# Performance work log

Hardware: AMD Instinct MI355X
Metric: run time of the kernel (lower is better)

Reference implementation:

```python
import jax, jax.numpy as jnp
import numpy as np

E = 256   # hidden_dim
H = 2     # num_heads
DH = E // H
EPS = 1e-5


def setup_inputs() -> dict:
    key = jax.random.key(0)
    ks = jax.random.split(key, 20)
    L, S, MAXLOOP = 8192, 8192, 16
    rel = jax.random.randint(ks[0], (L, MAXLOOP), 0, S)
    # sprinkle some padding sentinels (-1 / -2) like real edge loops
    pad = jax.random.uniform(ks[1], (L, MAXLOOP)) < 0.25
    rel = jnp.where(pad, -1, rel)
    rel = rel.at[:, 0].set(jnp.abs(rel[:, 0]) % S)  # ensure >=1 valid edge per face
    inp = {
        'v_face_edge_loop': rel.astype(jnp.int64) if jax.config.jax_enable_x64 else rel.astype(jnp.int32),
        'v_face_mask': jnp.ones((L,), dtype=bool),
        'v_edge_embedding': jax.random.normal(ks[2], (S, E), jnp.float32),
        'v_face_embedding': jax.random.normal(ks[3], (L, E), jnp.float32),
    }
    def w(k, shape):
        return (jax.random.normal(k, shape, jnp.float32) * 0.02)
    for i, base in ((1, 4), (2, 10)):
        inp[f'w_in{i}'] = w(ks[base + 0], (3 * E, E))
        inp[f'b_in{i}'] = jnp.zeros((3 * E,), jnp.float32)
        inp[f'w_out{i}'] = w(ks[base + 1], (E, E))
        inp[f'b_out{i}'] = jnp.zeros((E,), jnp.float32)
        inp[f'ln{i}_g'] = jnp.ones((E,), jnp.float32)
        inp[f'ln{i}_b'] = jnp.zeros((E,), jnp.float32)
    return inp


def _build_mask(face_edge_loop, S):
    # True = disallowed (torch bool attn_mask semantics).
    L = face_edge_loop.shape[0]
    rel = face_edge_loop
    invalid = (rel == -1) | (rel == -2)
    rel = jnp.where(invalid, S, rel)  # scatter invalids into sentinel column S
    mask = jnp.ones((L, S + 1), dtype=bool)
    mask = mask.at[jnp.arange(L)[:, None], rel].set(False)
    return mask[:, :S]  # [L, S]


def _mha(x, kv, mask, w_in, b_in, w_out, b_out):
    # torch nn.MultiheadAttention (unbatched, eval/no-dropout)
    wq, wk, wv = jnp.split(w_in, 3, axis=0)
    bq, bk, bv = jnp.split(b_in, 3, axis=0)
    L, S = x.shape[0], kv.shape[0]
    q = (x @ wq.T + bq).reshape(L, H, DH)
    k = (kv @ wk.T + bk).reshape(S, H, DH)
    v = (kv @ wv.T + bv).reshape(S, H, DH)
    scores = jnp.einsum('lhd,shd->hls', q, k) / np.sqrt(DH).astype(np.float32)
    scores = jnp.where(mask[None, :, :], jnp.float32(-1e9), scores)
    attn = jax.nn.softmax(scores, axis=-1)          # [H, L, S]
    out = jnp.einsum('hls,shd->lhd', attn, v).reshape(L, E)
    return out @ w_out.T + b_out


def _layernorm(x, g, b):
    m = x.mean(-1, keepdims=True)
    var = ((x - m) ** 2).mean(-1, keepdims=True)
    return (x - m) / jnp.sqrt(var + EPS) * g + b


def reference(v_face_edge_loop, v_face_mask, v_edge_embedding, v_face_embedding,
              w_in1, b_in1, w_out1, b_out1, ln1_g, ln1_b,
              w_in2, b_in2, w_out2, b_out2, ln2_g, ln2_b):
    S = v_edge_embedding.shape[0]
    # v_face_mask is all-True here (static shapes); loop[mask] == loop
    mask = _build_mask(v_face_edge_loop, S)
    x = v_face_embedding
    x = x + _mha(x, v_edge_embedding, mask, w_in1, b_in1, w_out1, b_out1)
    x = _layernorm(x, ln1_g, ln1_b)
    x = x + _mha(x, v_edge_embedding, mask, w_in2, b_in2, w_out2, b_out2)
    x = _layernorm(x, ln2_g, ln2_b)
    return x
```

## Files before the change

### kernel.cpp

```cpp
#include <hip/hip_runtime.h>
#include <hip/hip_bf16.h>

typedef short short8 __attribute__((ext_vector_type(8)));
typedef short short4v __attribute__((ext_vector_type(4)));
typedef float f32x4 __attribute__((ext_vector_type(4)));

#define E 256
#define DH 128

__device__ __forceinline__ float bf2f(__hip_bfloat16 x) { return __bfloat162float(x); }
__device__ __forceinline__ __hip_bfloat16 f2bf(float x) { return __float2bfloat16(x); }

struct CvtArgs { const float* in[6]; __hip_bfloat16* out[6]; int n[6]; };

__global__ __launch_bounds__(256) void f2b_all(CvtArgs a)
{
    int seg = blockIdx.y;
    int i = (blockIdx.x * 256 + threadIdx.x) * 8;
    if (i >= a.n[seg]) return;
    const float* in = a.in[seg];
    float4 x = *reinterpret_cast<const float4*>(in + i);
    float4 y = *reinterpret_cast<const float4*>(in + i + 4);
    __hip_bfloat16* o = a.out[seg] + i;
    o[0] = f2bf(x.x); o[1] = f2bf(x.y); o[2] = f2bf(x.z); o[3] = f2bf(x.w);
    o[4] = f2bf(y.x); o[5] = f2bf(y.y); o[6] = f2bf(y.z); o[7] = f2bf(y.w);
}

struct ProjSeg { const __hip_bfloat16* A; const __hip_bfloat16* W; const float* b; __hip_bfloat16* out; };
struct ProjArgs { ProjSeg seg[5]; };

#define GLDS(g, l) __builtin_amdgcn_global_load_lds( \
    (const __attribute__((address_space(1))) void*)(g), \
    (__attribute__((address_space(3))) void*)(l), 16, 0, 0)

__global__ __launch_bounds__(256) void gemm_proj(ProjArgs args, int M)
{
    __shared__ __hip_bfloat16 sA[2][32 * 64];
    __shared__ __hip_bfloat16 sW[2][256 * 64];

    int wv = threadIdx.x >> 6, lane = threadIdx.x & 63;
    int m0 = blockIdx.x * 32;
    ProjSeg sg = args.seg[blockIdx.y];
    int lo = lane & 15, hi = lane >> 4;

    int lr = lane >> 3;
    int lcol = ((lane & 7) ^ lr) * 8;

    auto stage = [&](int buf, int kc) {
        {
            int R = wv * 8 + lr;
            GLDS(sg.A + (size_t)(m0 + R) * E + kc * 64 + lcol, &sA[buf][(wv * 8) * 64]);
        }
#pragma unroll
        for (int s = 0; s < 8; ++s) {
            int R = wv * 64 + s * 8 + lr;
            GLDS(sg.W + (size_t)R * E + kc * 64 + lcol, &sW[buf][(wv * 64 + s * 8) * 64]);
        }
    };

    stage(0, 0);
    __syncthreads();

    f32x4 acc[2][4] = {};
    const int swz = (lo & 7);
#pragma unroll
    for (int kc = 0; kc < 4; ++kc) {
        int cur = kc & 1;
        if (kc < 3) stage(cur ^ 1, kc + 1);

        const char* aB = (const char*)sA[cur];
        const char* wB = (const char*)sW[cur];
#pragma unroll
        for (int ks = 0; ks < 2; ++ks) {
            int phys = ((hi + 4 * ks) ^ swz) * 16;
            short8 a0 = *reinterpret_cast<const short8*>(aB + (0 * 16 + lo) * 128 + phys);
            short8 a1 = *reinterpret_cast<const short8*>(aB + (1 * 16 + lo) * 128 + phys);
#pragma unroll
            for (int nt = 0; nt < 4; ++nt) {
                short8 b = *reinterpret_cast<const short8*>(
                    wB + (wv * 64 + nt * 16 + lo) * 128 + phys);
                acc[0][nt] = __builtin_amdgcn_mfma_f32_16x16x32_bf16(a0, b, acc[0][nt], 0, 0, 0);
                acc[1][nt] = __builtin_amdgcn_mfma_f32_16x16x32_bf16(a1, b, acc[1][nt], 0, 0, 0);
            }
        }
        __syncthreads();
    }

#pragma unroll
    for (int nt = 0; nt < 4; ++nt) {
        int col = wv * 64 + nt * 16 + lo;
        float bias = sg.b[col];
#pragma unroll
        for (int mt = 0; mt < 2; ++mt)
#pragma unroll
            for (int r = 0; r < 4; ++r) {
                int row = m0 + mt * 16 + hi * 4 + r;
                sg.out[(size_t)row * E + col] = f2bf(acc[mt][nt][r] + bias);
            }
    }
}

__global__ __launch_bounds__(1024) void attn_outproj_ln(
    const int* __restrict__ rel, const __hip_bfloat16* __restrict__ q16,
    const __hip_bfloat16* __restrict__ k16, const __hip_bfloat16* __restrict__ v16,
    const __hip_bfloat16* __restrict__ wout, const float* __restrict__ bout,
    const float* __restrict__ resid, const float* __restrict__ lng, const float* __restrict__ lnb,
    const __hip_bfloat16* __restrict__ wq_next, const float* __restrict__ bq_next,
    float* __restrict__ xres_out, __hip_bfloat16* __restrict__ qnext_out,
    float* __restrict__ final_out, int L, int ML)
{
    __shared__ __align__(16) __hip_bfloat16 atile[16 * 264];
    __shared__ __align__(16) float sm[16 * 260];
    __shared__ __align__(16) float lds_w[16][2][16];
    __shared__ int lds_idx[16][16];

    int tid = threadIdx.x, wv = tid >> 6, lane = tid & 63;
    int m0 = blockIdx.x * 16;
    int g = lane >> 2, q = lane & 3;
    int face = m0 + wv;
    const float scale = 0.088388347648318447f;

    const int* rr = rel + (size_t)face * ML;
    int myidx = (g < ML) ? rr[g] : -1;

    bool dup = false;
#pragma unroll
    for (int d = 1; d < 16; ++d) {
        int other = __shfl(myidx, ((g - d) & 15) * 4 + q);
        if (d <= g && other == myidx) dup = true;
    }
    bool myuse = (myidx >= 0) && !dup;
    int safe = myidx < 0 ? 0 : myidx;
    if (q == 0) lds_idx[wv][g] = safe;

#pragma unroll
    for (int h = 0; h < 2; ++h) {
        const __hip_bfloat16* kbase = k16 + (size_t)safe * E + h * DH;
        const __hip_bfloat16* qbase = q16 + (size_t)face * E + h * DH;
        float part = 0.f;
#pragma unroll
        for (int t = 0; t < 4; ++t) {
            short8 qv = *reinterpret_cast<const short8*>(qbase + (t * 4 + q) * 8);
            short8 kv = *reinterpret_cast<const short8*>(kbase + (t * 4 + q) * 8);
            const __hip_bfloat16* qp = (const __hip_bfloat16*)&qv;
            const __hip_bfloat16* kp = (const __hip_bfloat16*)&kv;
#pragma unroll
            for (int e2 = 0; e2 < 8; ++e2)
                part += bf2f(qp[e2]) * bf2f(kp[e2]);
        }
        part += __shfl_xor(part, 1);
        part += __shfl_xor(part, 2);
        float sc = myuse ? part * scale : -1e30f;
        float mx = sc;
#pragma unroll
        for (int off = 4; off < 64; off <<= 1) mx = fmaxf(mx, __shfl_xor(mx, off));
        float e = __expf(sc - mx);
        float den = e;
#pragma unroll
        for (int off = 4; off < 64; off <<= 1) den += __shfl_xor(den, off);
        if (q == 0) lds_w[wv][h][g] = e / den;
    }

    {
        int h = lane >> 5;
        float a0 = 0.f, a1 = 0.f, a2 = 0.f, a3 = 0.f;
#pragma unroll
        for (int j = 0; j < 16; ++j) {
            int ij = lds_idx[wv][j];
            float wj = lds_w[wv][h][j];
            short4v vv = *reinterpret_cast<const short4v*>(v16 + (size_t)ij * E + 4 * lane);
            const __hip_bfloat16* vp = (const __hip_bfloat16*)&vv;
            a0 += wj * bf2f(vp[0]);
            a1 += wj * bf2f(vp[1]);
            a2 += wj * bf2f(vp[2]);
            a3 += wj * bf2f(vp[3]);
        }
        __hip_bfloat16 ob[4] = {f2bf(a0), f2bf(a1), f2bf(a2), f2bf(a3)};
        *reinterpret_cast<short4v*>(atile + wv * 264 + 4 * lane) =
            *reinterpret_cast<const short4v*>(ob);
    }
    __syncthreads();

    {
        int lo = lane & 15, hi = lane >> 4;
        const __hip_bfloat16* arow = atile + lo * 264 + hi * 8;
        const __hip_bfloat16* brow = wout + (size_t)(wv * 16 + lo) * E + hi * 8;
        f32x4 acc = {0.f, 0.f, 0.f, 0.f};
#pragma unroll
        for (int kk = 0; kk < 8; ++kk) {
            short8 a = *reinterpret_cast<const short8*>(arow + kk * 32);
            short8 b = *reinterpret_cast<const short8*>(brow + kk * 32);
            acc = __builtin_amdgcn_mfma_f32_16x16x32_bf16(a, b, acc, 0, 0, 0);
        }
        int col = wv * 16 + lo;
#pragma unroll
        for (int r = 0; r < 4; ++r)
            sm[(hi * 4 + r) * 260 + col] = acc[r];
    }
    __syncthreads();

    {
        int rowg = m0 + wv;
        float4 pv = *reinterpret_cast<const float4*>(sm + wv * 260 + 4 * lane);
        float4 rv = *reinterpret_cast<const float4*>(resid + (size_t)rowg * E + 4 * lane);
        float4 bb = *reinterpret_cast<const float4*>(bout + 4 * lane);
        float v0 = pv.x + bb.x + rv.x;
        float v1 = pv.y + bb.y + rv.y;
        float v2 = pv.z + bb.z + rv.z;
        float v3 = pv.w + bb.w + rv.w;
        float s  = v0 + v1 + v2 + v3;
        float s2 = v0 * v0 + v1 * v1 + v2 * v2 + v3 * v3;
#pragma unroll
        for (int off = 1; off < 64; off <<= 1) {
            s  += __shfl_xor(s, off);
            s2 += __shfl_xor(s2, off);
        }
        float mean = s * (1.f / 256.f);
        float var  = s2 * (1.f / 256.f) - mean * mean;
        float rstd = rsqrtf(var + 1e-5f);
        float4 gg = *reinterpret_cast<const float4*>(lng + 4 * lane);
        float4 b2 = *reinterpret_cast<const float4*>(lnb + 4 * lane);
        float y0 = (v0 - mean) * rstd * gg.x + b2.x;
        float y1 = (v1 - mean) * rstd * gg.y + b2.y;
        float y2 = (v2 - mean) * rstd * gg.z + b2.z;
        float y3 = (v3 - mean) * rstd * gg.w + b2.w;
        if (final_out) {
            float4 o = {y0, y1, y2, y3};
            *reinterpret_cast<float4*>(final_out + (size_t)rowg * E + 4 * lane) = o;
        } else {
            float4 o = {y0, y1, y2, y3};
            *reinterpret_cast<float4*>(xres_out + (size_t)rowg * E + 4 * lane) = o;
            __hip_bfloat16 ob[4] = {f2bf(y0), f2bf(y1), f2bf(y2), f2bf(y3)};
            *reinterpret_cast<short4v*>(atile + wv * 264 + 4 * lane) =
                *reinterpret_cast<const short4v*>(ob);
        }
    }

    if (qnext_out) {
        __syncthreads();
        int lo = lane & 15, hi = lane >> 4;
        const __hip_bfloat16* arow = atile + lo * 264 + hi * 8;
        const __hip_bfloat16* brow = wq_next + (size_t)(wv * 16 + lo) * E + hi * 8;
        f32x4 acc = {0.f, 0.f, 0.f, 0.f};
#pragma unroll
        for (int kk = 0; kk < 8; ++kk) {
            short8 a = *reinterpret_cast<const short8*>(arow + kk * 32);
            short8 b = *reinterpret_cast<const short8*>(brow + kk * 32);
            acc = __builtin_amdgcn_mfma_f32_16x16x32_bf16(a, b, acc, 0, 0, 0);
        }
        int col = wv * 16 + lo;
        float bias = bq_next[col];
#pragma unroll
        for (int r = 0; r < 4; ++r)
            qnext_out[(size_t)(m0 + hi * 4 + r) * E + col] = f2bf(acc[r] + bias);
    }
}

extern "C" void kernel_launch(void* const* d_in, const int* in_sizes, int n_in,
                              void* d_out, int out_size, void* d_ws, size_t ws_size,
                              hipStream_t stream) {
    const int* rel = (const int*)d_in[0];
    const float* edge = (const float*)d_in[2];
    const float* face = (const float*)d_in[3];
    const float* w_in[2]  = {(const float*)d_in[4],  (const float*)d_in[10]};
    const float* b_in[2]  = {(const float*)d_in[5],  (const float*)d_in[11]};
    const float* w_out[2] = {(const float*)d_in[6],  (const float*)d_in[12]};
    const float* b_out[2] = {(const float*)d_in[7],  (const float*)d_in[13]};
    const float* ln_g[2]  = {(const float*)d_in[8],  (const float*)d_in[14]};
    const float* ln_b[2]  = {(const float*)d_in[9],  (const float*)d_in[15]};

    int S = in_sizes[2] / E;
    int L = in_sizes[3] / E;
    int ML = in_sizes[0] / L;

    char* ws = (char*)d_ws;
    __hip_bfloat16* face16 = (__hip_bfloat16*)ws; ws += (size_t)L * E * 2;
    __hip_bfloat16* edge16 = (__hip_bfloat16*)ws; ws += (size_t)S * E * 2;
    __hip_bfloat16* q16    = (__hip_bfloat16*)ws; ws += (size_t)L * E * 2;
    __hip_bfloat16* k16[2], *v16[2];
    for (int l = 0; l < 2; ++l) {
        k16[l] = (__hip_bfloat16*)ws; ws += (size_t)S * E * 2;
        v16[l] = (__hip_bfloat16*)ws; ws += (size_t)S * E * 2;
    }
    float* xres = (float*)ws;                     ws += (size_t)L * E * 4;
    __hip_bfloat16* win16[2], *wout16[2];
    for (int l = 0; l < 2; ++l) {
        win16[l]  = (__hip_bfloat16*)ws; ws += (size_t)3 * E * E * 2;
        wout16[l] = (__hip_bfloat16*)ws; ws += (size_t)E * E * 2;
    }

    float* outp = (float*)d_out;

    {
        CvtArgs ca;
        ca.in[0] = face;     ca.out[0] = face16;    ca.n[0] = L * E;
        ca.in[1] = edge;     ca.out[1] = edge16;    ca.n[1] = S * E;
        ca.in[2] = w_in[0];  ca.out[2] = win16[0];  ca.n[2] = 3 * E * E;
        ca.in[3] = w_in[1];  ca.out[3] = win16[1];  ca.n[3] = 3 * E * E;
        ca.in[4] = w_out[0]; ca.out[4] = wout16[0]; ca.n[4] = E * E;
        ca.in[5] = w_out[1]; ca.out[5] = wout16[1]; ca.n[5] = E * E;
        int gx = (L * E) / (256 * 8);
        f2b_all<<<dim3(gx, 6), 256, 0, stream>>>(ca);
    }

    {
        ProjArgs pa;
        pa.seg[0] = {face16, win16[0],                     b_in[0],         q16};
        pa.seg[1] = {edge16, win16[0] + (size_t)E * E,     b_in[0] + E,     k16[0]};
        pa.seg[2] = {edge16, win16[0] + (size_t)2 * E * E, b_in[0] + 2 * E, v16[0]};
        pa.seg[3] = {edge16, win16[1] + (size_t)E * E,     b_in[1] + E,     k16[1]};
        pa.seg[4] = {edge16, win16[1] + (size_t)2 * E * E, b_in[1] + 2 * E, v16[1]};
        gemm_proj<<<dim3(L / 32, 5), 256, 0, stream>>>(pa, L);
    }

    attn_outproj_ln<<<L / 16, 1024, 0, stream>>>(rel, q16, k16[0], v16[0],
                                                 wout16[0], b_out[0], face,
                                                 ln_g[0], ln_b[0],
                                                 win16[1], b_in[1],
                                                 xres, q16, nullptr, L, ML);

    attn_outproj_ln<<<L / 16, 1024, 0, stream>>>(rel, q16, k16[1], v16[1],
                                                 wout16[1], b_out[1], xres,
                                                 ln_g[1], ln_b[1],
                                                 nullptr, nullptr,
                                                 nullptr, nullptr, outp, L, ML);
}
```

Measured before the change: 167.9 us.

## Fuse both attention layers into one kernel keeping residual and Q in registers/LDS

Merges the two attention+outproj+layernorm launches into a single kernel. The layer-1 LN output stays in registers as the residual, and the next-layer Q projection is written to an LDS tile instead of global memory. The gather indices and dedup mask are reused across both layers. This removes a launch plus the xres fp32 and q16 round trips through global memory, at the cost of more LDS per block and a longer kernel.

```diff
diff --git a/kernel.cpp b/kernel.cpp
--- a/kernel.cpp
+++ b/kernel.cpp
@@ -100,16 +100,19 @@
     }
 }
 
-__global__ __launch_bounds__(1024) void attn_outproj_ln(
+__global__ __launch_bounds__(1024) void attn2_fused(
     const int* __restrict__ rel, const __hip_bfloat16* __restrict__ q16,
-    const __hip_bfloat16* __restrict__ k16, const __hip_bfloat16* __restrict__ v16,
-    const __hip_bfloat16* __restrict__ wout, const float* __restrict__ bout,
-    const float* __restrict__ resid, const float* __restrict__ lng, const float* __restrict__ lnb,
-    const __hip_bfloat16* __restrict__ wq_next, const float* __restrict__ bq_next,
-    float* __restrict__ xres_out, __hip_bfloat16* __restrict__ qnext_out,
-    float* __restrict__ final_out, int L, int ML)
+    const __hip_bfloat16* __restrict__ k0, const __hip_bfloat16* __restrict__ v0,
+    const __hip_bfloat16* __restrict__ wout0, const float* __restrict__ bout0,
+    const float* __restrict__ resid0, const float* __restrict__ ln0g, const float* __restrict__ ln0b,
+    const __hip_bfloat16* __restrict__ wq1, const float* __restrict__ bq1,
+    const __hip_bfloat16* __restrict__ k1, const __hip_bfloat16* __restrict__ v1,
+    const __hip_bfloat16* __restrict__ wout1, const float* __restrict__ bout1,
+    const float* __restrict__ ln1g, const float* __restrict__ ln1b,
+    float* __restrict__ out, int L, int ML)
 {
     __shared__ __align__(16) __hip_bfloat16 atile[16 * 264];
+    __shared__ __align__(16) __hip_bfloat16 qtile[16 * 264];
     __shared__ __align__(16) float sm[16 * 260];
     __shared__ __align__(16) float lds_w[16][2][16];
     __shared__ int lds_idx[16][16];
@@ -118,6 +121,7 @@
     int m0 = blockIdx.x * 16;
     int g = lane >> 2, q = lane & 3;
     int face = m0 + wv;
+    int lo = lane & 15, hi = lane >> 4;
     const float scale = 0.088388347648318447f;
 
     const int* rr = rel + (size_t)face * ML;
@@ -135,7 +139,7 @@
 
 #pragma unroll
     for (int h = 0; h < 2; ++h) {
-        const __hip_bfloat16* kbase = k16 + (size_t)safe * E + h * DH;
+        const __hip_bfloat16* kbase = k0 + (size_t)safe * E + h * DH;
         const __hip_bfloat16* qbase = q16 + (size_t)face * E + h * DH;
         float part = 0.f;
 #pragma unroll
@@ -168,7 +172,7 @@
         for (int j = 0; j < 16; ++j) {
             int ij = lds_idx[wv][j];
             float wj = lds_w[wv][h][j];
-            short4v vv = *reinterpret_cast<const short4v*>(v16 + (size_t)ij * E + 4 * lane);
+            short4v vv = *reinterpret_cast<const short4v*>(v0 + (size_t)ij * E + 4 * lane);
             const __hip_bfloat16* vp = (const __hip_bfloat16*)&vv;
             a0 += wj * bf2f(vp[0]);
             a1 += wj * bf2f(vp[1]);
@@ -182,9 +186,8 @@
     __syncthreads();
 
     {
-        int lo = lane & 15, hi = lane >> 4;
         const __hip_bfloat16* arow = atile + lo * 264 + hi * 8;
-        const __hip_bfloat16* brow = wout + (size_t)(wv * 16 + lo) * E + hi * 8;
+        const __hip_bfloat16* brow = wout0 + (size_t)(wv * 16 + lo) * E + hi * 8;
         f32x4 acc = {0.f, 0.f, 0.f, 0.f};
 #pragma unroll
         for (int kk = 0; kk < 8; ++kk) {
@@ -199,17 +202,17 @@
     }
     __syncthreads();
 
-    {
-        int rowg = m0 + wv;
+    float y0, y1, y2, y3;
+    {
         float4 pv = *reinterpret_cast<const float4*>(sm + wv * 260 + 4 * lane);
-        float4 rv = *reinterpret_cast<const float4*>(resid + (size_t)rowg * E + 4 * lane);
-        float4 bb = *reinterpret_cast<const float4*>(bout + 4 * lane);
-        float v0 = pv.x + bb.x + rv.x;
-        float v1 = pv.y + bb.y + rv.y;
-        float v2 = pv.z + bb.z + rv.z;
-        float v3 = pv.w + bb.w + rv.w;
-        float s  = v0 + v1 + v2 + v3;
-        float s2 = v0 * v0 + v1 * v1 + v2 * v2 + v3 * v3;
+        float4 rv = *reinterpret_cast<const float4*>(resid0 + (size_t)face * E + 4 * lane);
+        float4 bb = *reinterpret_cast<const float4*>(bout0 + 4 * lane);
+        float v0_ = pv.x + bb.x + rv.x;
+        float v1_ = pv.y + bb.y + rv.y;
+        float v2_ = pv.z + bb.z + rv.z;
+        float v3_ = pv.w + bb.w + rv.w;
+        float s  = v0_ + v1_ + v2_ + v3_;
+        float s2 = v0_ * v0_ + v1_ * v1_ + v2_ * v2_ + v3_ * v3_;
 #pragma unroll
         for (int off = 1; off < 64; off <<= 1) {
             s  += __shfl_xor(s, off);
@@ -218,29 +221,21 @@
         float mean = s * (1.f / 256.f);
         float var  = s2 * (1.f / 256.f) - mean * mean;
         float rstd = rsqrtf(var + 1e-5f);
-        float4 gg = *reinterpret_cast<const float4*>(lng + 4 * lane);
-        float4 b2 = *reinterpret_cast<const float4*>(lnb + 4 * lane);
-        float y0 = (v0 - mean) * rstd * gg.x + b2.x;
-        float y1 = (v1 - mean) * rstd * gg.y + b2.y;
-        float y2 = (v2 - mean) * rstd * gg.z + b2.z;
-        float y3 = (v3 - mean) * rstd * gg.w + b2.w;
-        if (final_out) {
-            float4 o = {y0, y1, y2, y3};
-            *reinterpret_cast<float4*>(final_out + (size_t)rowg * E + 4 * lane) = o;
-        } else {
-            float4 o = {y0, y1, y2, y3};
-            *reinterpret_cast<float4*>(xres_out + (size_t)rowg * E + 4 * lane) = o;
-            __hip_bfloat16 ob[4] = {f2bf(y0), f2bf(y1), f2bf(y2), f2bf(y3)};
-            *reinterpret_cast<short4v*>(atile + wv * 264 + 4 * lane) =
-                *reinterpret_cast<const short4v*>(ob);
-        }
-    }
-
-    if (qnext_out) {
-        __syncthreads();
-        int lo = lane & 15, hi = lane >> 4;
+        float4 gg = *reinterpret_cast<const float4*>(ln0g + 4 * lane);
+        float4 b2 = *reinterpret_cast<const float4*>(ln0b + 4 * lane);
+        y0 = (v0_ - mean) * rstd * gg.x + b2.x;
+        y1 = (v1_ - mean) * rstd * gg.y + b2.y;
+        y2 = (v2_ - mean) * rstd * gg.z + b2.z;
+        y3 = (v3_ - mean) * rstd * gg.w + b2.w;
+        __hip_bfloat16 ob[4] = {f2bf(y0), f2bf(y1), f2bf(y2), f2bf(y3)};
+        *reinterpret_cast<short4v*>(atile + wv * 264 + 4 * lane) =
+            *reinterpret_cast<const short4v*>(ob);
+    }
+    __syncthreads();
+
+    {
         const __hip_bfloat16* arow = atile + lo * 264 + hi * 8;
-        const __hip_bfloat16* brow = wq_next + (size_t)(wv * 16 + lo) * E + hi * 8;
+        const __hip_bfloat16* brow = wq1 + (size_t)(wv * 16 + lo) * E + hi * 8;
         f32x4 acc = {0.f, 0.f, 0.f, 0.f};
 #pragma unroll
         for (int kk = 0; kk < 8; ++kk) {
@@ -249,10 +244,103 @@
             acc = __builtin_amdgcn_mfma_f32_16x16x32_bf16(a, b, acc, 0, 0, 0);
         }
         int col = wv * 16 + lo;
-        float bias = bq_next[col];
+        float bias = bq1[col];
 #pragma unroll
         for (int r = 0; r < 4; ++r)
-            qnext_out[(size_t)(m0 + hi * 4 + r) * E + col] = f2bf(acc[r] + bias);
+            qtile[(hi * 4 + r) * 264 + col] = f2bf(acc[r] + bias);
+    }
+    __syncthreads();
+
+#pragma unroll
+    for (int h = 0; h < 2; ++h) {
+        const __hip_bfloat16* kbase = k1 + (size_t)safe * E + h * DH;
+        const __hip_bfloat16* qbase = qtile + wv * 264 + h * DH;
+        float part = 0.f;
+#pragma unroll
+        for (int t = 0; t < 4; ++t) {
+            short8 qv = *reinterpret_cast<const short8*>(qbase + (t * 4 + q) * 8);
+            short8 kv = *reinterpret_cast<const short8*>(kbase + (t * 4 + q) * 8);
+            const __hip_bfloat16* qp = (const __hip_bfloat16*)&qv;
+            const __hip_bfloat16* kp = (const __hip_bfloat16*)&kv;
+#pragma unroll
+            for (int e2 = 0; e2 < 8; ++e2)
+                part += bf2f(qp[e2]) * bf2f(kp[e2]);
+        }
+        part += __shfl_xor(part, 1);
+        part += __shfl_xor(part, 2);
+        float sc = myuse ? part * scale : -1e30f;
+        float mx = sc;
+#pragma unroll
+        for (int off = 4; off < 64; off <<= 1) mx = fmaxf(mx, __shfl_xor(mx, off));
+        float e = __expf(sc - mx);
+        float den = e;
+#pragma unroll
+        for (int off = 4; off < 64; off <<= 1) den += __shfl_xor(den, off);
+        if (q == 0) lds_w[wv][h][g] = e / den;
+    }
+
+    {
+        int h = lane >> 5;
+        float a0 = 0.f, a1 = 0.f, a2 = 0.f, a3 = 0.f;
+#pragma unroll
+        for (int j = 0; j < 16; ++j) {
+            int ij = lds_idx[wv][j];
+            float wj = lds_w[wv][h][j];
+            short4v vv = *reinterpret_cast<const short4v*>(v1 + (size_t)ij * E + 4 * lane);
+            const __hip_bfloat16* vp = (const __hip_bfloat16*)&vv;
+            a0 += wj * bf2f(vp[0]);
+            a1 += wj * bf2f(vp[1]);
+            a2 += wj * bf2f(vp[2]);
+            a3 += wj * bf2f(vp[3]);
+        }
+        __hip_bfloat16 ob[4] = {f2bf(a0), f2bf(a1), f2bf(a2), f2bf(a3)};
+        *reinterpret_cast<short4v*>(atile + wv * 264 + 4 * lane) =
+            *reinterpret_cast<const short4v*>(ob);
+    }
+    __syncthreads();
+
+    {
+        const __hip_bfloat16* arow = atile + lo * 264 + hi * 8;
+        const __hip_bfloat16* brow = wout1 + (size_t)(wv * 16 + lo) * E + hi * 8;
+        f32x4 acc = {0.f, 0.f, 0.f, 0.f};
+#pragma unroll
+        for (int kk = 0; kk < 8; ++kk) {
+            short8 a = *reinterpret_cast<const short8*>(arow + kk * 32);
+            short8 b = *reinterpret_cast<const short8*>(brow + kk * 32);
+            acc = __builtin_amdgcn_mfma_f32_16x16x32_bf16(a, b, acc, 0, 0, 0);
+        }
+        int col = wv * 16 + lo;
+#pragma unroll
+        for (int r = 0; r < 4; ++r)
+            sm[(hi * 4 + r) * 260 + col] = acc[r];
+    }
+    __syncthreads();
+
+    {
+        float4 pv = *reinterpret_cast<const float4*>(sm + wv * 260 + 4 * lane);
+        float4 bb = *reinterpret_cast<const float4*>(bout1 + 4 * lane);
+        float v0_ = pv.x + bb.x + y0;
+        float v1_ = pv.y + bb.y + y1;
+        float v2_ = pv.z + bb.z + y2;
+        float v3_ = pv.w + bb.w + y3;
+        float s  = v0_ + v1_ + v2_ + v3_;
+        float s2 = v0_ * v0_ + v1_ * v1_ + v2_ * v2_ + v3_ * v3_;
+#pragma unroll
+        for (int off = 1; off < 64; off <<= 1) {
+            s  += __shfl_xor(s, off);
+            s2 += __shfl_xor(s2, off);
+        }
+        float mean = s * (1.f / 256.f);
+        float var  = s2 * (1.f / 256.f) - mean * mean;
+        float rstd = rsqrtf(var + 1e-5f);
+        float4 gg = *reinterpret_cast<const float4*>(ln1g + 4 * lane);
+        float4 b2 = *reinterpret_cast<const float4*>(ln1b + 4 * lane);
+        float4 o;
+        o.x = (v0_ - mean) * rstd * gg.x + b2.x;
+        o.y = (v1_ - mean) * rstd * gg.y + b2.y;
+        o.z = (v2_ - mean) * rstd * gg.z + b2.z;
+        o.w = (v3_ - mean) * rstd * gg.w + b2.w;
+        *reinterpret_cast<float4*>(out + (size_t)face * E + 4 * lane) = o;
     }
 }
 
@@ -282,7 +370,6 @@
         k16[l] = (__hip_bfloat16*)ws; ws += (size_t)S * E * 2;
         v16[l] = (__hip_bfloat16*)ws; ws += (size_t)S * E * 2;
     }
-    float* xres = (float*)ws;                     ws += (size_t)L * E * 4;
     __hip_bfloat16* win16[2], *wout16[2];
     for (int l = 0; l < 2; ++l) {
         win16[l]  = (__hip_bfloat16*)ws; ws += (size_t)3 * E * E * 2;
@@ -313,15 +400,12 @@
         gemm_proj<<<dim3(L / 32, 5), 256, 0, stream>>>(pa, L);
     }
 
-    attn_outproj_ln<<<L / 16, 1024, 0, stream>>>(rel, q16, k16[0], v16[0],
-                                                 wout16[0], b_out[0], face,
-                                                 ln_g[0], ln_b[0],
-                                                 win16[1], b_in[1],
-                                                 xres, q16, nullptr, L, ML);
-
-    attn_outproj_ln<<<L / 16, 1024, 0, stream>>>(rel, q16, k16[1], v16[1],
-                                                 wout16[1], b_out[1], xres,
-                                                 ln_g[1], ln_b[1],
-                                                 nullptr, nullptr,
-                                                 nullptr, nullptr, outp, L, ML);
+    attn2_fused<<<L / 16, 1024, 0, stream>>>(rel, q16, k16[0], v16[0],
+                                             wout16[0], b_out[0], face,
+                                             ln_g[0], ln_b[0],
+                                             win16[1], b_in[1],
+                                             k16[1], v16[1],
+                                             wout16[1], b_out[1],
+                                             ln_g[1], ln_b[1],
+                                             outp, L, ML);
 }
```

After: 171.0 us. About the same (+1.8%).
